# Optimization experiments

Measured on AMD Instinct MI355X. Metric: run time of the kernel, lower is better.

Reference implementation:

```python
import jax, jax.numpy as jnp
import numpy as np

B, S, H = 128, 256, 512


def setup_inputs() -> dict:
    key = jax.random.key(0)
    ks = jax.random.split(key, 20)
    sc = 0.02
    inp = {
        "facts": jax.random.normal(ks[0], (B, S, H), jnp.float32),
        "questions": jax.random.normal(ks[1], (B, 1, H), jnp.float32),
        "prevM": jax.random.normal(ks[2], (B, 1, H), jnp.float32),
        # interaction gate MLP: z1 (4H->H), z2 (H->1)
        "z1_w": jax.random.normal(ks[3], (4 * H, H), jnp.float32) * sc,
        "z1_b": jnp.zeros((H,), jnp.float32),
        "z2_w": jax.random.normal(ks[4], (H, 1), jnp.float32) * sc,
        "z2_b": jnp.zeros((1,), jnp.float32),
        # AttentionGRUCell params (input_size = hidden_size = H)
        "Wr": jax.random.normal(ks[5], (H, H), jnp.float32) * sc,
        "br": jnp.zeros((H,), jnp.float32),
        "Ur": jax.random.normal(ks[6], (H, H), jnp.float32) * sc,
        "bur": jnp.zeros((H,), jnp.float32),
        "W": jax.random.normal(ks[7], (H, H), jnp.float32) * sc,
        "bw": jnp.zeros((H,), jnp.float32),
        "U": jax.random.normal(ks[8], (H, H), jnp.float32) * sc,
        "bu": jnp.zeros((H,), jnp.float32),
        # next memory projection (3H -> H)
        "nm_w": jax.random.normal(ks[9], (3 * H, H), jnp.float32) * sc,
        "nm_b": jnp.zeros((H,), jnp.float32),
    }
    return inp


def _episodic_memory(facts, questions, prevM,
                     z1_w, z1_b, z2_w, z2_b,
                     Wr, br, Ur, bur, W, bw, U, bu,
                     nm_w, nm_b):
    # ---- make_interaction ----
    q = questions  # (B,1,H) broadcasts against (B,S,H)
    m = prevM
    z = jnp.concatenate(
        [facts * q, facts * m, jnp.abs(facts - q), jnp.abs(facts - m)],
        axis=2,
    )  # (B,S,4H)
    g_hidden = jnp.tanh(jnp.einsum("bsf,fh->bsh", z, z1_w) + z1_b)
    G_logits = (jnp.einsum("bsh,ho->bso", g_hidden, z2_w) + z2_b)[..., 0]  # (B,S)
    G = jax.nn.softmax(G_logits, axis=1)  # (B,S)

    # ---- AttentionGRU scan over sentences ----
    pre_r = jnp.einsum("bsh,hk->bsh", facts, Wr) + br  # Wr @ fact, all steps
    pre_h = jnp.einsum("bsh,hk->bsh", facts, W) + bw   # W  @ fact, all steps

    def step(C, xs):
        pr, ph, g = xs  # (B,H), (B,H), (B,)
        r = jax.nn.sigmoid(pr + C @ Ur + bur)
        h_tilda = jnp.tanh(ph + r * (C @ U + bu))
        g = g[:, None]
        return g * h_tilda + (1.0 - g) * C, None

    C0 = jnp.zeros((facts.shape[0], Wr.shape[1]), facts.dtype)
    xs = (jnp.swapaxes(pre_r, 0, 1), jnp.swapaxes(pre_h, 0, 1), G.T)  # lead S
    C, _ = jax.lax.scan(step, C0, xs)  # (B,H)

    # ---- next memory ----
    concat = jnp.concatenate([prevM[:, 0], C, questions[:, 0]], axis=1)  # (B,3H)
    next_mem = jax.nn.relu(concat @ nm_w + nm_b)
    return next_mem[:, None, :]  # (B,1,H)


def reference(facts, questions, prevM, z1_w, z1_b, z2_w, z2_b,
              Wr, br, Ur, bur, W, bw, U, bu, nm_w, nm_b):
    return _episodic_memory(facts, questions, prevM, z1_w, z1_b, z2_w, z2_b,
                            Wr, br, Ur, bur, W, bw, U, bu, nm_w, nm_b)
```

## Files before the change

### kernel.cpp

```cpp
#include <hip/hip_runtime.h>
#include <stdint.h>

#define B_ 128
#define S_ 256
#define H_ 512

typedef __attribute__((ext_vector_type(4))) float f32x4;
typedef __attribute__((ext_vector_type(4))) int i32x4;
typedef __attribute__((ext_vector_type(2))) unsigned int u32x2;
typedef __attribute__((ext_vector_type(8))) __bf16 bf16x8;
typedef unsigned long long u64;

#define OFF_G      0
#define OFF_RSR    131072
#define OFF_RSH    133120
#define OFF_FLG    135168
#define OFF_EX     139264
#define OFF_CBUF   401408
#define OFF_LOGITS 401408
#define OFF_BP     663552
#define OFF_PB     2760704

__device__ __forceinline__ unsigned short f2bf(float f) {
  unsigned u = __builtin_bit_cast(unsigned, f);
  u += 0x7FFFu + ((u >> 16) & 1u);
  return (unsigned short)(u >> 16);
}
__device__ __forceinline__ float fast_sigmoid(float x) {
  return 1.0f / (1.0f + __expf(-x));
}
__device__ __forceinline__ float fast_tanh(float x) {
  return 1.0f - 2.0f / (__expf(2.0f * x) + 1.0f);
}

__global__ void k_prep_bp(const float* __restrict__ z1w,
                          unsigned short* __restrict__ Bp) {
  int t = blockIdx.x * blockDim.x + threadIdx.x;
  int k = t >> 9, n = t & 511;
  Bp[((k >> 3) * 512 + n) * 8 + (k & 7)] = f2bf(z1w[t]);
}

__global__ void k_prep_pb(const float* __restrict__ Ur,
                          const float* __restrict__ U,
                          unsigned short* __restrict__ PB) {
  int t = blockIdx.x * blockDim.x + threadIdx.x;
  int j = t & 7;
  int l = (t >> 3) & 63;
  int kt = (t >> 9) & 15;
  int w = (t >> 13) & 7;
  int mem = t >> 16;
  int k = kt * 32 + ((l >> 4) & 3) * 8 + j;
  int n = mem * 64 + (w & 3) * 16 + (l & 15);
  const float* src = (w >> 2) ? U : Ur;
  PB[t] = f2bf(src[k * 512 + n]);
}

__global__ void k_prep_rs(const float* __restrict__ Wr,
                          const float* __restrict__ W,
                          float* __restrict__ rsr, float* __restrict__ rsh) {
  __shared__ float red[4];
  int h2 = blockIdx.x;
  int t = threadIdx.x;
  const float* M = (h2 >= 512) ? W : Wr;
  int h = h2 & 511;
  float sv = M[h * 512 + t] + M[h * 512 + 256 + t];
#pragma unroll
  for (int mask = 1; mask < 64; mask <<= 1) sv += __shfl_xor(sv, mask, 64);
  if ((t & 63) == 0) red[t >> 6] = sv;
  __syncthreads();
  if (t == 0) {
    float tot = red[0] + red[1] + red[2] + red[3];
    ((h2 >= 512) ? rsh : rsr)[h] = tot;
  }
}

__global__ __launch_bounds__(512, 4) void k_gate(
    const float* __restrict__ facts, const float* __restrict__ questions,
    const float* __restrict__ prevM, const float* __restrict__ z1b,
    const float* __restrict__ z2w, const unsigned short* __restrict__ Bp,
    float* __restrict__ logits) {
  __shared__ float qS[512], mS[512], z1bS[512], z2wS[512];
  __shared__ unsigned short At[64 * 40];
  __shared__ unsigned short Bt[16384];
  __shared__ float lp[64 * 4];
  const int tid = threadIdx.x;
  const int row0 = blockIdx.x * 64;
  const int b = row0 >> 8;
  const int s0 = row0 & 255;
  qS[tid] = questions[b * 512 + tid];
  mS[tid] = prevM[b * 512 + tid];
  z1bS[tid] = z1b[tid];
  z2wS[tid] = z2w[tid];
  const int w = tid >> 6, l = tid & 63;
  const int mgrp = w & 1, ngrp = w >> 1;
  const int lm = l & 15, lk = l >> 4;
  f32x4 acc[2][8];
#pragma unroll
  for (int a = 0; a < 2; ++a)
#pragma unroll
    for (int i = 0; i < 8; ++i) acc[a][i] = (f32x4){0.f, 0.f, 0.f, 0.f};
  const int arow = tid >> 3, ac = tid & 7;
  const float* fbase = facts + ((size_t)(b * 256 + s0 + arow)) * 512 + ac * 4;

  for (int kb = 0; kb < 64; ++kb) {
    __syncthreads();
    const int part = kb >> 4;
    const int h0 = (kb & 15) * 32;
    f32x4 fv = *(const f32x4*)(fbase + h0);
    f32x4 ov = (part & 1) ? *(const f32x4*)&mS[h0 + ac * 4]
                          : *(const f32x4*)&qS[h0 + ac * 4];
    float z0, z1, z2, z3;
    if (part < 2) {
      z0 = fv[0] * ov[0]; z1 = fv[1] * ov[1];
      z2 = fv[2] * ov[2]; z3 = fv[3] * ov[3];
    } else {
      z0 = fabsf(fv[0] - ov[0]); z1 = fabsf(fv[1] - ov[1]);
      z2 = fabsf(fv[2] - ov[2]); z3 = fabsf(fv[3] - ov[3]);
    }
    unsigned p0 = (unsigned)f2bf(z0) | ((unsigned)f2bf(z1) << 16);
    unsigned p1 = (unsigned)f2bf(z2) | ((unsigned)f2bf(z3) << 16);
    u32x2 pk = {p0, p1};
    *(u32x2*)&At[arow * 40 + ac * 4] = pk;
    const char* bsrc = (const char*)Bp + (size_t)kb * 32768;
#pragma unroll
    for (int i = 0; i < 4; ++i)
      *(i32x4*)((char*)Bt + i * 8192 + tid * 16) =
          *(const i32x4*)(bsrc + i * 8192 + tid * 16);
    __syncthreads();
    bf16x8 af[2];
#pragma unroll
    for (int mi = 0; mi < 2; ++mi) {
      i32x4 av = *(const i32x4*)&At[((mgrp * 2 + mi) * 16 + lm) * 40 + lk * 8];
      af[mi] = __builtin_bit_cast(bf16x8, av);
    }
#pragma unroll
    for (int i = 0; i < 8; ++i) {
      const int nt = ngrp * 8 + i;
      i32x4 bv = *(const i32x4*)&Bt[lk * 4096 + (nt * 16 + lm) * 8];
      bf16x8 bf = __builtin_bit_cast(bf16x8, bv);
      acc[0][i] = __builtin_amdgcn_mfma_f32_16x16x32_bf16(af[0], bf, acc[0][i], 0, 0, 0);
      acc[1][i] = __builtin_amdgcn_mfma_f32_16x16x32_bf16(af[1], bf, acc[1][i], 0, 0, 0);
    }
  }
  float pr_[2][4];
#pragma unroll
  for (int mi = 0; mi < 2; ++mi)
#pragma unroll
    for (int r = 0; r < 4; ++r) pr_[mi][r] = 0.f;
#pragma unroll
  for (int i = 0; i < 8; ++i) {
    const int n_i = (ngrp * 8 + i) * 16 + lm;
    const float zb = z1bS[n_i], zw = z2wS[n_i];
#pragma unroll
    for (int mi = 0; mi < 2; ++mi)
#pragma unroll
      for (int r = 0; r < 4; ++r)
        pr_[mi][r] += fast_tanh(acc[mi][i][r] + zb) * zw;
  }
#pragma unroll
  for (int mask = 1; mask < 16; mask <<= 1)
#pragma unroll
    for (int mi = 0; mi < 2; ++mi)
#pragma unroll
      for (int r = 0; r < 4; ++r)
        pr_[mi][r] += __shfl_xor(pr_[mi][r], mask, 64);
  if (lm == 0) {
#pragma unroll
    for (int mi = 0; mi < 2; ++mi)
#pragma unroll
      for (int r = 0; r < 4; ++r)
        lp[((mgrp * 2 + mi) * 16 + lk * 4 + r) * 4 + ngrp] = pr_[mi][r];
  }
  __syncthreads();
  if (tid < 64)
    logits[row0 + tid] =
        lp[tid * 4] + lp[tid * 4 + 1] + lp[tid * 4 + 2] + lp[tid * 4 + 3];
}

__global__ void k_softmax(const float* __restrict__ logits,
                          float* __restrict__ G) {
  __shared__ float red[4], red2[4];
  int b = blockIdx.x, t = threadIdx.x;
  float v = logits[b * 256 + t];
  float mx = v;
#pragma unroll
  for (int mask = 1; mask < 64; mask <<= 1)
    mx = fmaxf(mx, __shfl_xor(mx, mask, 64));
  if ((t & 63) == 0) red[t >> 6] = mx;
  __syncthreads();
  mx = fmaxf(fmaxf(red[0], red[1]), fmaxf(red[2], red[3]));
  float e = __expf(v - mx);
  float sm = e;
#pragma unroll
  for (int mask = 1; mask < 64; mask <<= 1) sm += __shfl_xor(sm, mask, 64);
  if ((t & 63) == 0) red2[t >> 6] = sm;
  __syncthreads();
  sm = red2[0] + red2[1] + red2[2] + red2[3];
  G[b * 256 + t] = e / sm;
}

__global__ __launch_bounds__(512, 1) void k_scan(
    const float* __restrict__ facts, const float* __restrict__ Gm,
    const unsigned short* __restrict__ PB, const float* __restrict__ rsr,
    const float* __restrict__ rsh, const float* __restrict__ br,
    const float* __restrict__ bur, const float* __restrict__ bw,
    const float* __restrict__ bu, u64* __restrict__ EXq,
    unsigned int* __restrict__ FLG, float* __restrict__ Cb) {
  __shared__ unsigned short A[16 * 520];
  __shared__ float outb[8 * 272];
  const int tid = threadIdx.x;
  const int g = blockIdx.x & 7;
  const int mem = blockIdx.x >> 3;
  const int w = tid >> 6, l = tid & 63;
  const int lm = l & 15, lk = (l >> 4) & 3;
  for (int i = tid; i < 16 * 520 / 4; i += 512) ((u64*)A)[i] = 0ull;
  i32x4 bfr[16];
  const char* pb = (const char*)PB + (size_t)(mem * 8 + w) * 16384;
#pragma unroll
  for (int kt = 0; kt < 16; ++kt)
    bfr[kt] = *(const i32x4*)(pb + kt * 1024 + l * 16);
  const int bb = tid >> 4;
  const int nq = tid & 15;
  const int n0 = mem * 64 + nq * 4;
  const int batch = g * 16 + bb;
  f32x4 c_rsr, c_br, c_rsh, c_bw, c_bur, c_bu;
  const float* fptr = nullptr;
  const float* gptr = nullptr;
  if (tid < 256) {
    c_rsr = *(const f32x4*)(rsr + n0);
    c_br  = *(const f32x4*)(br + n0);
    c_rsh = *(const f32x4*)(rsh + n0);
    c_bw  = *(const f32x4*)(bw + n0);
    c_bur = *(const f32x4*)(bur + n0);
    c_bu  = *(const f32x4*)(bu + n0);
    fptr = facts + (size_t)batch * 256 * 512 + n0;
    gptr = Gm + batch * 256;
  }
  const int pollmem = (tid < mem) ? tid : tid + 1;
  f32x4 Cv = (f32x4){0.f, 0.f, 0.f, 0.f};
  __syncthreads();

  for (int s = 0; s < 256; ++s) {
    const unsigned tag = (unsigned)(s + 1);
    const unsigned base = ((unsigned)(s & 1) * 8 + (unsigned)g) * 2048;
    f32x4 fct;
    float gval = 0.f;
    if (tid < 256) {
      fct = *(const f32x4*)(fptr + (size_t)s * 512);
      gval = gptr[s];
    }
    f32x4 acc0 = (f32x4){0.f, 0.f, 0.f, 0.f};
    f32x4 acc1 = (f32x4){0.f, 0.f, 0.f, 0.f};
#pragma unroll
    for (int kt = 0; kt < 16; ++kt) {
      i32x4 av = *(const i32x4*)&A[lm * 520 + kt * 32 + lk * 8];
      bf16x8 afv = __builtin_bit_cast(bf16x8, av);
      bf16x8 bfv = __builtin_bit_cast(bf16x8, bfr[kt]);
      if (kt & 1)
        acc1 = __builtin_amdgcn_mfma_f32_16x16x32_bf16(afv, bfv, acc1, 0, 0, 0);
      else
        acc0 = __builtin_amdgcn_mfma_f32_16x16x32_bf16(afv, bfv, acc0, 0, 0, 0);
    }
    f32x4 accs = acc0 + acc1;
#pragma unroll
    for (int r = 0; r < 4; ++r)
      outb[w * 272 + (lk * 4 + r) * 17 + lm] = accs[r];
    __syncthreads();
    if (tid < 256) {
      unsigned short pk[4];
#pragma unroll
      for (int r = 0; r < 4; ++r) {
        const int n_loc = nq * 4 + r;
        const float uro = outb[(n_loc >> 4) * 272 + bb * 17 + (n_loc & 15)];
        const float uuo = outb[(4 + (n_loc >> 4)) * 272 + bb * 17 + (n_loc & 15)];
        const float pr = fct[r] * c_rsr[r] + c_br[r];
        const float ph = fct[r] * c_rsh[r] + c_bw[r];
        const float r_ = fast_sigmoid(pr + uro + c_bur[r]);
        const float ht = fast_tanh(ph + r_ * (uuo + c_bu[r]));
        Cv[r] = gval * ht + (1.0f - gval) * Cv[r];
        pk[r] = f2bf(Cv[r]);
      }
      const u64 word = (u64)pk[0] | ((u64)pk[1] << 16) | ((u64)pk[2] << 32) |
                       ((u64)pk[3] << 48);
      *(u64*)((char*)A + bb * 1040 + n0 * 2) = word;
      __hip_atomic_store(EXq + base + (unsigned)bb * 128 + (unsigned)(n0 >> 2),
                         word, __ATOMIC_RELAXED, __HIP_MEMORY_SCOPE_AGENT);
    }
    __syncthreads();
    if (tid == 0)
      __hip_atomic_store(FLG + g * 8 + mem, tag, __ATOMIC_RELAXED,
                         __HIP_MEMORY_SCOPE_AGENT);
    if (tid < 7) {
      int guard = 0;
      for (;;) {
        unsigned v = __hip_atomic_load(FLG + g * 8 + pollmem, __ATOMIC_RELAXED,
                                       __HIP_MEMORY_SCOPE_AGENT);
        if (v >= tag) break;
        __builtin_amdgcn_s_sleep(1);
        if (++guard > (1 << 22)) break;
      }
    }
    __syncthreads();
    const u64* srcq = EXq + base;
#pragma unroll
    for (int i = 0; i < 4; ++i) {
      const int u = tid * 4 + i;
      const int nu = u & 127;
      if ((nu >> 4) != mem) {
        u64 wv = __hip_atomic_load(srcq + u, __ATOMIC_RELAXED,
                                   __HIP_MEMORY_SCOPE_AGENT);
        *(u64*)((char*)A + (u >> 7) * 1040 + nu * 8) = wv;
      }
    }
    __syncthreads();
  }
  if (tid < 256) *(f32x4*)(Cb + (size_t)batch * 512 + n0) = Cv;
}

__global__ __launch_bounds__(512) void k_final(
    const float* __restrict__ prevM, const float* __restrict__ questions,
    const float* __restrict__ Cb, const float* __restrict__ nmw,
    const float* __restrict__ nmb, float* __restrict__ out) {
  __shared__ float cc[2][1536];
  const int t = threadIdx.x;
  const int b0 = blockIdx.x * 2;
  for (int i = t; i < 1536; i += 512) {
#pragma unroll
    for (int bi = 0; bi < 2; ++bi) {
      int bbx = b0 + bi;
      float v;
      if (i < 512) v = prevM[bbx * 512 + i];
      else if (i < 1024) v = Cb[bbx * 512 + i - 512];
      else v = questions[bbx * 512 + i - 1024];
      cc[bi][i] = v;
    }
  }
  __syncthreads();
  const int h = t;
  float a0 = nmb[h], a1 = nmb[h];
#pragma unroll 4
  for (int f = 0; f < 1536; ++f) {
    float wv = nmw[f * 512 + h];
    a0 = fmaf(cc[0][f], wv, a0);
    a1 = fmaf(cc[1][f], wv, a1);
  }
  out[(size_t)b0 * 512 + h] = fmaxf(a0, 0.f);
  out[(size_t)(b0 + 1) * 512 + h] = fmaxf(a1, 0.f);
}

extern "C" void kernel_launch(void* const* d_in, const int* in_sizes, int n_in,
                              void* d_out, int out_size, void* d_ws,
                              size_t ws_size, hipStream_t stream) {
  const float* facts     = (const float*)d_in[0];
  const float* questions = (const float*)d_in[1];
  const float* prevM     = (const float*)d_in[2];
  const float* z1w       = (const float*)d_in[3];
  const float* z1b       = (const float*)d_in[4];
  const float* z2w       = (const float*)d_in[5];
  const float* Wr        = (const float*)d_in[7];
  const float* br        = (const float*)d_in[8];
  const float* Ur        = (const float*)d_in[9];
  const float* bur       = (const float*)d_in[10];
  const float* W         = (const float*)d_in[11];
  const float* bw        = (const float*)d_in[12];
  const float* U         = (const float*)d_in[13];
  const float* bu        = (const float*)d_in[14];
  const float* nmw       = (const float*)d_in[15];
  const float* nmb       = (const float*)d_in[16];

  char* ws = (char*)d_ws;
  float* G             = (float*)(ws + OFF_G);
  float* rsr           = (float*)(ws + OFF_RSR);
  float* rsh           = (float*)(ws + OFF_RSH);
  unsigned* FLG        = (unsigned*)(ws + OFF_FLG);
  u64* EXq             = (u64*)(ws + OFF_EX);
  float* Cb            = (float*)(ws + OFF_CBUF);
  float* logits        = (float*)(ws + OFF_LOGITS);
  unsigned short* Bp   = (unsigned short*)(ws + OFF_BP);
  unsigned short* PB   = (unsigned short*)(ws + OFF_PB);

  hipMemsetAsync(FLG, 0, 64 * sizeof(unsigned), stream);
  k_prep_bp<<<2048, 512, 0, stream>>>(z1w, Bp);
  k_prep_pb<<<1024, 512, 0, stream>>>(Ur, U, PB);
  k_prep_rs<<<1024, 256, 0, stream>>>(Wr, W, rsr, rsh);
  k_gate<<<512, 512, 0, stream>>>(facts, questions, prevM, z1b, z2w, Bp, logits);
  k_softmax<<<128, 256, 0, stream>>>(logits, G);
  k_scan<<<64, 512, 0, stream>>>(facts, G, PB, rsr, rsh, br, bur, bw, bu, EXq,
                                 FLG, Cb);
  k_final<<<64, 512, 0, stream>>>(prevM, questions, Cb, nmw, nmb, (float*)d_out);
}
```

Baseline: 1.033 ms.

## Replace flag-based cross-block barrier with tagged per-element exchange words

```diff
diff --git a/kernel.cpp b/kernel.cpp
--- a/kernel.cpp
+++ b/kernel.cpp
@@ -14,12 +14,11 @@
 #define OFF_G      0
 #define OFF_RSR    131072
 #define OFF_RSH    133120
-#define OFF_FLG    135168
-#define OFF_EX     139264
-#define OFF_CBUF   401408
-#define OFF_LOGITS 401408
-#define OFF_BP     663552
-#define OFF_PB     2760704
+#define OFF_EX     135168
+#define OFF_BP     659456
+#define OFF_CBUF   659456
+#define OFF_PB     2756608
+#define OFF_LOGITS 3805184
 
 __device__ __forceinline__ unsigned short f2bf(float f) {
   unsigned u = __builtin_bit_cast(unsigned, f);
@@ -204,8 +203,8 @@
     const unsigned short* __restrict__ PB, const float* __restrict__ rsr,
     const float* __restrict__ rsh, const float* __restrict__ br,
     const float* __restrict__ bur, const float* __restrict__ bw,
-    const float* __restrict__ bu, u64* __restrict__ EXq,
-    unsigned int* __restrict__ FLG, float* __restrict__ Cb) {
+    const float* __restrict__ bu, unsigned int* __restrict__ EX,
+    float* __restrict__ Cb) {
   __shared__ unsigned short A[16 * 520];
   __shared__ float outb[8 * 272];
   const int tid = threadIdx.x;
@@ -236,13 +235,14 @@
     fptr = facts + (size_t)batch * 256 * 512 + n0;
     gptr = Gm + batch * 256;
   }
-  const int pollmem = (tid < mem) ? tid : tid + 1;
+  const bool ownCol = ((tid >> 6) == mem);
+  unsigned short* colA = (unsigned short*)((char*)A + tid * 2);
   f32x4 Cv = (f32x4){0.f, 0.f, 0.f, 0.f};
   __syncthreads();
 
   for (int s = 0; s < 256; ++s) {
     const unsigned tag = (unsigned)(s + 1);
-    const unsigned base = ((unsigned)(s & 1) * 8 + (unsigned)g) * 2048;
+    const unsigned base = ((unsigned)(s & 1) * 8 + (unsigned)g) * 8192;
     f32x4 fct;
     float gval = 0.f;
     if (tid < 256) {
@@ -280,36 +280,50 @@
         Cv[r] = gval * ht + (1.0f - gval) * Cv[r];
         pk[r] = f2bf(Cv[r]);
       }
+      const u64 q0 = (u64)(((unsigned)pk[0] << 16) | tag) |
+                     ((u64)(((unsigned)pk[1] << 16) | tag) << 32);
+      const u64 q1 = (u64)(((unsigned)pk[2] << 16) | tag) |
+                     ((u64)(((unsigned)pk[3] << 16) | tag) << 32);
+      u64* dst = (u64*)(EX + base + (unsigned)bb * 512 + (unsigned)n0);
+      __hip_atomic_store(dst, q0, __ATOMIC_RELAXED, __HIP_MEMORY_SCOPE_AGENT);
+      __hip_atomic_store(dst + 1, q1, __ATOMIC_RELAXED, __HIP_MEMORY_SCOPE_AGENT);
       const u64 word = (u64)pk[0] | ((u64)pk[1] << 16) | ((u64)pk[2] << 32) |
                        ((u64)pk[3] << 48);
       *(u64*)((char*)A + bb * 1040 + n0 * 2) = word;
-      __hip_atomic_store(EXq + base + (unsigned)bb * 128 + (unsigned)(n0 >> 2),
-                         word, __ATOMIC_RELAXED, __HIP_MEMORY_SCOPE_AGENT);
-    }
-    __syncthreads();
-    if (tid == 0)
-      __hip_atomic_store(FLG + g * 8 + mem, tag, __ATOMIC_RELAXED,
-                         __HIP_MEMORY_SCOPE_AGENT);
-    if (tid < 7) {
+    }
+    if (!ownCol) {
+      const unsigned* src = EX + base + (unsigned)tid;
+      if (tid >= 256) __builtin_amdgcn_s_sleep(4);
+      unsigned vbuf[16];
+#pragma unroll
+      for (int i = 0; i < 16; ++i)
+        vbuf[i] = __hip_atomic_load(src + i * 512, __ATOMIC_RELAXED,
+                                    __HIP_MEMORY_SCOPE_AGENT);
+      unsigned pending = 0;
+#pragma unroll
+      for (int i = 0; i < 16; ++i) {
+        if ((vbuf[i] & 0xFFFFu) == tag)
+          colA[i * 520] = (unsigned short)(vbuf[i] >> 16);
+        else
+          pending |= 1u << i;
+      }
       int guard = 0;
-      for (;;) {
-        unsigned v = __hip_atomic_load(FLG + g * 8 + pollmem, __ATOMIC_RELAXED,
-                                       __HIP_MEMORY_SCOPE_AGENT);
-        if (v >= tag) break;
+      while (pending) {
         __builtin_amdgcn_s_sleep(1);
+        unsigned np = pending;
+#pragma unroll
+        for (int i = 0; i < 16; ++i) {
+          if ((np >> i) & 1u) {
+            unsigned v = __hip_atomic_load(src + i * 512, __ATOMIC_RELAXED,
+                                           __HIP_MEMORY_SCOPE_AGENT);
+            if ((v & 0xFFFFu) == tag) {
+              colA[i * 520] = (unsigned short)(v >> 16);
+              np &= ~(1u << i);
+            }
+          }
+        }
+        pending = np;
         if (++guard > (1 << 22)) break;
-      }
-    }
-    __syncthreads();
-    const u64* srcq = EXq + base;
-#pragma unroll
-    for (int i = 0; i < 4; ++i) {
-      const int u = tid * 4 + i;
-      const int nu = u & 127;
-      if ((nu >> 4) != mem) {
-        u64 wv = __hip_atomic_load(srcq + u, __ATOMIC_RELAXED,
-                                   __HIP_MEMORY_SCOPE_AGENT);
-        *(u64*)((char*)A + (u >> 7) * 1040 + nu * 8) = wv;
       }
     }
     __syncthreads();
@@ -372,20 +386,17 @@
   float* G             = (float*)(ws + OFF_G);
   float* rsr           = (float*)(ws + OFF_RSR);
   float* rsh           = (float*)(ws + OFF_RSH);
-  unsigned* FLG        = (unsigned*)(ws + OFF_FLG);
-  u64* EXq             = (u64*)(ws + OFF_EX);
+  unsigned* EX         = (unsigned*)(ws + OFF_EX);
   float* Cb            = (float*)(ws + OFF_CBUF);
   float* logits        = (float*)(ws + OFF_LOGITS);
   unsigned short* Bp   = (unsigned short*)(ws + OFF_BP);
   unsigned short* PB   = (unsigned short*)(ws + OFF_PB);
 
-  hipMemsetAsync(FLG, 0, 64 * sizeof(unsigned), stream);
   k_prep_bp<<<2048, 512, 0, stream>>>(z1w, Bp);
   k_prep_pb<<<1024, 512, 0, stream>>>(Ur, U, PB);
   k_prep_rs<<<1024, 256, 0, stream>>>(Wr, W, rsr, rsh);
   k_gate<<<512, 512, 0, stream>>>(facts, questions, prevM, z1b, z2w, Bp, logits);
   k_softmax<<<128, 256, 0, stream>>>(logits, G);
-  k_scan<<<64, 512, 0, stream>>>(facts, G, PB, rsr, rsh, br, bur, bw, bu, EXq,
-                                 FLG, Cb);
+  k_scan<<<64, 512, 0, stream>>>(facts, G, PB, rsr, rsh, br, bur, bw, bu, EX, Cb);
   k_final<<<64, 512, 0, stream>>>(prevM, questions, Cb, nmw, nmb, (float*)d_out);
 }
```

New measurement: 1.603 ms. +55.2%, slower.
